# Performance work log

Hardware: AMD Instinct MI355X
Metric: run time of the kernel (lower is better)

## Reference

```python
import jax, jax.numpy as jnp
import numpy as np

N = 20000          # graph_size
IN_DIM = 256
H, D = 3, 64       # num_heads (hardcoded 3 in source), out_dim
E = 640000         # N * avg_degree(32)
NEG_SLOPE = 0.2    # DGL GATConv default negative_slope


def setup_inputs() -> dict:
    key = jax.random.key(0)
    ks = jax.random.split(key, 8)
    feat = jax.random.normal(ks[0], (N, IN_DIM), dtype=jnp.float32)
    W = jax.random.normal(ks[1], (IN_DIM, H * D), dtype=jnp.float32) * 0.05
    attn_l = jax.random.normal(ks[2], (H, D), dtype=jnp.float32) * 0.05
    attn_r = jax.random.normal(ks[3], (H, D), dtype=jnp.float32) * 0.05
    gat_bias = jnp.zeros((H * D,), dtype=jnp.float32)
    fc_w = jax.random.normal(ks[4], (N * H * D, 2), dtype=jnp.float32) * 0.001
    fc_b = jnp.zeros((2,), dtype=jnp.float32)
    src = jax.random.randint(ks[5], (E,), 0, N, dtype=jnp.int64)
    dst = jax.random.randint(ks[6], (E,), 0, N, dtype=jnp.int64)
    return {"feat": feat, "W": W, "attn_l": attn_l, "attn_r": attn_r,
            "gat_bias": gat_bias, "fc_w": fc_w, "fc_b": fc_b,
            "src": src, "dst": dst}


def reference(feat, W, attn_l, attn_r, gat_bias, fc_w, fc_b, src, dst):
    n = feat.shape[0]
    # GATConv: projected multi-head features [N, H, D]
    h = (feat @ W).reshape(n, H, D)
    el = jnp.einsum('nhd,hd->nh', h, attn_l)   # [N, H]
    er = jnp.einsum('nhd,hd->nh', h, attn_r)   # [N, H]
    # per-edge raw attention logits, LeakyReLU(el[src] + er[dst])
    e = jax.nn.leaky_relu(el[src] + er[dst], negative_slope=NEG_SLOPE)  # [E, H]
    # edge-softmax grouped by destination node (stable)
    m = jax.ops.segment_max(e, dst, num_segments=n)   # [N, H]
    ex = jnp.exp(e - m[dst])
    denom = jax.ops.segment_sum(ex, dst, num_segments=n)  # [N, H]
    alpha = ex / denom[dst]                            # [E, H]
    # weighted message aggregation: out[v] = sum_{(u->v)} alpha * h[u]
    msg = h[src] * alpha[:, :, None]                   # [E, H, D]
    out = jax.ops.segment_sum(msg, dst, num_segments=n)  # [N, H, D]
    out = out + gat_bias.reshape(H, D)                 # GATConv bias
    out = jax.nn.relu(out)                             # self.activation
    # Flatten(start_dim=0) -> Linear(N*H*D, 2)
    return out.reshape(-1) @ fc_w + fc_b               # [2]
```

## Files before the change

### kernel.cpp

```cpp
#include <hip/hip_runtime.h>
#include <hip/hip_bf16.h>
#include <cstdint>
#include <cstddef>

#define INDIM  256
#define HD     192
#define NHEADS 3
#define NEG_SLOPE 0.2f
#define ELLPAD 96
#define LPAD   97
#define CSHIFT 7
#define NBUCK  160
#define BCAP   4608
#define FNODES 16
#define P1CHUNK 2048

typedef __attribute__((ext_vector_type(8))) short short8;
typedef __attribute__((ext_vector_type(4))) float f32x4;

__device__ __forceinline__ float wave_sum(float v) {
#pragma unroll
    for (int o = 32; o; o >>= 1) v += __shfl_xor(v, o, 64);
    return v;
}

__global__ __launch_bounds__(256) void prep_kernel(
    const float* __restrict__ W, __hip_bfloat16* __restrict__ Wt,
    int* __restrict__ gCur)
{
    const int b = blockIdx.x, tid = threadIdx.x;
    if (b == 0) {
        if (tid < NBUCK) gCur[tid] = 0;
        return;
    }
    int n = b - 1;
    Wt[n * 256 + tid] = __float2bfloat16(W[tid * HD + n]);
}

__global__ __launch_bounds__(256) void gemm_bucket_kernel(
    const float* __restrict__ feat,
    const __hip_bfloat16* __restrict__ Wt,
    const float* __restrict__ attn_l, const float* __restrict__ attn_r,
    __hip_bfloat16* __restrict__ hb, float* __restrict__ el,
    float* __restrict__ er, int M,
    const int* __restrict__ src, const int* __restrict__ dst,
    int* __restrict__ gCur, int2* __restrict__ pairs,
    int E, int gemmBlocks)
{
    const int tid = threadIdx.x;
    if (blockIdx.x >= gemmBlocks) {
        __shared__ int cnt[NBUCK];
        __shared__ int base[NBUCK];
        const int e0 = (blockIdx.x - gemmBlocks) * P1CHUNK;
        if (tid < NBUCK) cnt[tid] = 0;
        __syncthreads();
        int d[8], s[8], b[8], l[8];
#pragma unroll
        for (int u = 0; u < 8; u++) {
            int e = e0 + u * 256 + tid;
            if (e < E) {
                d[u] = dst[e]; s[u] = src[e];
                b[u] = d[u] >> CSHIFT;
                l[u] = atomicAdd(&cnt[b[u]], 1);
            } else b[u] = -1;
        }
        __syncthreads();
        if (tid < NBUCK && cnt[tid] > 0) base[tid] = atomicAdd(&gCur[tid], cnt[tid]);
        __syncthreads();
#pragma unroll
        for (int u = 0; u < 8; u++) {
            if (b[u] >= 0) {
                int idx = base[b[u]] + l[u];
                if (idx < BCAP)
                    pairs[(size_t)b[u] * BCAP + idx] = make_int2(d[u], s[u]);
            }
        }
        return;
    }
    __shared__ __hip_bfloat16 As[64][40];
    __shared__ __hip_bfloat16 Bs[192][40];
    const int lane = tid & 63, w = tid >> 6;
    const int q = lane >> 4, ll = lane & 15;
    const int row0 = blockIdx.x * 64;

    f32x4 acc[12];
#pragma unroll
    for (int c = 0; c < 12; c++) acc[c] = (f32x4){0.f, 0.f, 0.f, 0.f};

    const int sr = tid >> 2, sk = (tid & 3) * 8;
    const int grow = row0 + sr;
    const bool arow = grow < M;
    const float* ap = feat + (size_t)grow * INDIM + sk;
    const __hip_bfloat16* bp = Wt + (size_t)tid * INDIM;

    float4 a0 = make_float4(0.f, 0.f, 0.f, 0.f), a1 = a0;
    if (arow) { a0 = *(const float4*)ap; a1 = *(const float4*)(ap + 4); }
    uint4 b0, b1, b2, b3;
    if (tid < HD) {
        b0 = *(const uint4*)(bp);      b1 = *(const uint4*)(bp + 8);
        b2 = *(const uint4*)(bp + 16); b3 = *(const uint4*)(bp + 24);
    }

    for (int k0 = 0; k0 < INDIM; k0 += 32) {
        __hip_bfloat16 ab[8] = {__float2bfloat16(a0.x), __float2bfloat16(a0.y),
                                __float2bfloat16(a0.z), __float2bfloat16(a0.w),
                                __float2bfloat16(a1.x), __float2bfloat16(a1.y),
                                __float2bfloat16(a1.z), __float2bfloat16(a1.w)};
        __syncthreads();
        *(uint4*)&As[sr][sk] = *(const uint4*)ab;
        if (tid < HD) {
            *(uint4*)&Bs[tid][0]  = b0;
            *(uint4*)&Bs[tid][8]  = b1;
            *(uint4*)&Bs[tid][16] = b2;
            *(uint4*)&Bs[tid][24] = b3;
        }
        if (k0 + 32 < INDIM) {
            if (arow) {
                a0 = *(const float4*)(ap + k0 + 32);
                a1 = *(const float4*)(ap + k0 + 36);
            }
            if (tid < HD) {
                const __hip_bfloat16* bq = bp + k0 + 32;
                b0 = *(const uint4*)(bq);      b1 = *(const uint4*)(bq + 8);
                b2 = *(const uint4*)(bq + 16); b3 = *(const uint4*)(bq + 24);
            }
        }
        __syncthreads();

        short8 af = *(const short8*)&As[w * 16 + ll][q * 8];
#pragma unroll
        for (int c = 0; c < 12; c++) {
            short8 bf = *(const short8*)&Bs[c * 16 + ll][q * 8];
            acc[c] = __builtin_amdgcn_mfma_f32_16x16x32_bf16(af, bf, acc[c], 0, 0, 0);
        }
    }

    float al[12], ar[12];
#pragma unroll
    for (int c = 0; c < 12; c++) {
        al[c] = attn_l[c * 16 + ll];
        ar[c] = attn_r[c * 16 + ll];
    }
    float sl[3][4], sr_[3][4];
#pragma unroll
    for (int hd = 0; hd < 3; hd++)
#pragma unroll
        for (int i = 0; i < 4; i++) {
            float a = 0.f, b = 0.f;
#pragma unroll
            for (int f = 0; f < 4; f++) {
                a = fmaf(acc[hd * 4 + f][i], al[hd * 4 + f], a);
                b = fmaf(acc[hd * 4 + f][i], ar[hd * 4 + f], b);
            }
            sl[hd][i] = a; sr_[hd][i] = b;
        }
#pragma unroll
    for (int hd = 0; hd < 3; hd++)
#pragma unroll
        for (int i = 0; i < 4; i++)
#pragma unroll
            for (int off = 1; off < 16; off <<= 1) {
                sl[hd][i]  += __shfl_xor(sl[hd][i],  off, 64);
                sr_[hd][i] += __shfl_xor(sr_[hd][i], off, 64);
            }
#pragma unroll
    for (int c = 0; c < 12; c++)
#pragma unroll
        for (int i = 0; i < 4; i++) {
            int row = row0 + w * 16 + q * 4 + i;
            if (row < M)
                hb[(size_t)row * HD + c * 16 + ll] = __float2bfloat16(acc[c][i]);
        }
    if (ll == 0) {
#pragma unroll
        for (int i = 0; i < 4; i++) {
            int row = row0 + w * 16 + q * 4 + i;
            if (row < M) {
#pragma unroll
                for (int hd = 0; hd < 3; hd++) {
                    el[row * 4 + hd] = sl[hd][i];
                    er[row * 4 + hd] = sr_[hd][i];
                }
            }
        }
    }
}

__global__ __launch_bounds__(1024) void gat_bucket_kernel(
    const __hip_bfloat16* __restrict__ h, const float* __restrict__ el,
    const float* __restrict__ er, const int2* __restrict__ pairs,
    const int* __restrict__ gCur, const float* __restrict__ gbias,
    const float* __restrict__ fc_w, float* __restrict__ pA,
    float* __restrict__ pB, int N)
{
    __shared__ int cur[FNODES];
    __shared__ int lell[FNODES][LPAD];
    __shared__ float4 sE[16][64];

    const int bid = blockIdx.x;
    const int tid = threadIdx.x;
    const int lane = tid & 63, wslot = tid >> 6;
    const int cb = bid >> 3, sub = bid & 7;

    if (tid < FNODES) cur[tid] = 0;
    __syncthreads();
    const int pcnt = min(gCur[cb], BCAP);
    const int2* pp = pairs + (size_t)cb * BCAP;
    for (int i = tid; i < pcnt; i += 1024) {
        int2 p = pp[i];
        int nl = p.x & 127;
        if ((nl >> 4) == sub) {
            int f = nl & 15;
            int r = atomicAdd(&cur[f], 1);
            if (r < ELLPAD) lell[f][r] = p.y;
        }
    }
    __syncthreads();

    const int v = bid * FNODES + wslot;
    if (v >= N) return;

    const int cnt = min(cur[wslot], ELLPAD);
    const int* rowp = &lell[wslot][0];
    const float4 erv = ((const float4*)er)[v];
    const float er0 = erv.x, er1 = erv.y, er2 = erv.z;
    const __hip_bfloat16* hl = h + lane;

    float acc0 = 0.f, acc1 = 0.f, acc2 = 0.f;
    float d0 = 0.f, d1 = 0.f, d2 = 0.f;

    for (int chunk = 0; chunk < cnt; chunk += 64) {
        const int i = chunk + lane;
        float w0 = 0.f, w1 = 0.f, w2 = 0.f;
        int s = 0;
        if (i < cnt) {
            s = rowp[i];
            const float4 le = ((const float4*)el)[s];
            float l0 = le.x + er0;
            float l1 = le.y + er1;
            float l2 = le.z + er2;
            l0 = l0 > 0.f ? l0 : NEG_SLOPE * l0;
            l1 = l1 > 0.f ? l1 : NEG_SLOPE * l1;
            l2 = l2 > 0.f ? l2 : NEG_SLOPE * l2;
            w0 = __expf(l0); w1 = __expf(l1); w2 = __expf(l2);
        }
        d0 += w0; d1 += w1; d2 += w2;
        sE[wslot][lane] = make_float4(__int_as_float(s), w0, w1, w2);
        __asm__ volatile("s_waitcnt lgkmcnt(0)" ::: "memory");

        const int rem = min(cnt - chunk, 64);
        const int nR = (rem + 7) & ~7;
        for (int j = 0; j < nR; j += 8) {
            float4 e[8];
#pragma unroll
            for (int u = 0; u < 8; u++) e[u] = sE[wslot][j + u];
            float x0[8], x1[8], x2[8];
#pragma unroll
            for (int u = 0; u < 8; u++) {
                const __hip_bfloat16* p = hl + (size_t)__float_as_int(e[u].x) * HD;
                x0[u] = __bfloat162float(p[0]);
                x1[u] = __bfloat162float(p[64]);
                x2[u] = __bfloat162float(p[128]);
            }
#pragma unroll
            for (int u = 0; u < 8; u++) {
                acc0 = fmaf(e[u].y, x0[u], acc0);
                acc1 = fmaf(e[u].z, x1[u], acc1);
                acc2 = fmaf(e[u].w, x2[u], acc2);
            }
        }
    }

    d0 = wave_sum(d0); d1 = wave_sum(d1); d2 = wave_sum(d2);

    float o0 = (d0 > 0.f) ? acc0 / d0 : 0.f;
    float o1 = (d1 > 0.f) ? acc1 / d1 : 0.f;
    float o2 = (d2 > 0.f) ? acc2 / d2 : 0.f;
    o0 = fmaxf(o0 + gbias[lane], 0.f);
    o1 = fmaxf(o1 + gbias[64 + lane], 0.f);
    o2 = fmaxf(o2 + gbias[128 + lane], 0.f);

    const size_t bidx = (size_t)v * HD;
    float2 w0v = ((const float2*)fc_w)[bidx + lane];
    float2 w1v = ((const float2*)fc_w)[bidx + 64 + lane];
    float2 w2v = ((const float2*)fc_w)[bidx + 128 + lane];
    float f0 = fmaf(o0, w0v.x, fmaf(o1, w1v.x, o2 * w2v.x));
    float f1 = fmaf(o0, w0v.y, fmaf(o1, w1v.y, o2 * w2v.y));

    f0 = wave_sum(f0); f1 = wave_sum(f1);
    if (lane == 0) { pA[v] = f0; pB[v] = f1; }
}

__global__ __launch_bounds__(1024) void final_reduce(const float* __restrict__ pA,
                                                     const float* __restrict__ pB,
                                                     const float* __restrict__ fc_b,
                                                     float* __restrict__ out, int nb)
{
    int tid = threadIdx.x;
    float s0 = 0.f, s1 = 0.f;
    for (int i = tid; i < nb; i += 1024) { s0 += pA[i]; s1 += pB[i]; }
    s0 = wave_sum(s0); s1 = wave_sum(s1);
    __shared__ float sh[32];
    int lane = tid & 63, w = tid >> 6;
    if (lane == 0) { sh[w * 2] = s0; sh[w * 2 + 1] = s1; }
    __syncthreads();
    if (tid == 0) {
        float t0 = 0.f, t1 = 0.f;
#pragma unroll
        for (int i = 0; i < 16; i++) { t0 += sh[i * 2]; t1 += sh[i * 2 + 1]; }
        out[0] = t0 + fc_b[0];
        out[1] = t1 + fc_b[1];
    }
}

extern "C" void kernel_launch(void* const* d_in, const int* in_sizes, int n_in,
                              void* d_out, int out_size, void* d_ws, size_t ws_size,
                              hipStream_t stream)
{
    const float* feat   = (const float*)d_in[0];
    const float* W      = (const float*)d_in[1];
    const float* attn_l = (const float*)d_in[2];
    const float* attn_r = (const float*)d_in[3];
    const float* gbias  = (const float*)d_in[4];
    const float* fc_w   = (const float*)d_in[5];
    const float* fc_b   = (const float*)d_in[6];
    const int*   src    = (const int*)d_in[7];
    const int*   dst    = (const int*)d_in[8];

    const int N = in_sizes[0] / INDIM;
    const int E = in_sizes[7];
    const int nFine = (N + FNODES - 1) / FNODES;

    __hip_bfloat16* Wt = (__hip_bfloat16*)d_ws;
    __hip_bfloat16* hb = Wt + HD * INDIM;
    float* el = (float*)(hb + (size_t)N * HD);
    float* er = el + (size_t)N * 4;
    int* gCur = (int*)(er + (size_t)N * 4);
    int2* pairs = (int2*)(gCur + NBUCK);
    float* pA = (float*)(pairs + (size_t)NBUCK * BCAP);
    float* pB = pA + N;

    prep_kernel<<<1 + HD, 256, 0, stream>>>(W, Wt, gCur);

    const int gemmBlocks = (N + 63) / 64;
    const int p1Blocks = (E + P1CHUNK - 1) / P1CHUNK;
    gemm_bucket_kernel<<<gemmBlocks + p1Blocks, 256, 0, stream>>>(
        feat, Wt, attn_l, attn_r, hb, el, er, N,
        src, dst, gCur, pairs, E, gemmBlocks);

    gat_bucket_kernel<<<nFine, 1024, 0, stream>>>(hb, el, er, pairs, gCur,
                                                  gbias, fc_w, pA, pB, N);
    final_reduce<<<1, 1024, 0, stream>>>(pA, pB, fc_b, (float*)d_out, N);
}
```

Before: 165.5 us.

## Pack edge pairs into 32-bit words and widen gather unroll in GAT kernel

Each edge is now stored in the bucket buffer as a single 32-bit word, source index shifted left by 7 with the low 7 bits of the destination, instead of an int2. The aggregation kernel reads these words four at a time with uint4 loads and keeps the shared-memory adjacency list as 16-bit indices. This halves the bucket write and re-read traffic, which matters because each bucket is scanned by eight blocks. The fc_w loads are issued before the edge loop to hide their latency, and the feature gather is unrolled to 16 raw bf16 loads per step. The 16-bit adjacency indices only hold node ids below 65536, and the wider unroll raises register pressure.

```diff
diff --git a/kernel.cpp b/kernel.cpp
--- a/kernel.cpp
+++ b/kernel.cpp
@@ -8,7 +8,6 @@
 #define NHEADS 3
 #define NEG_SLOPE 0.2f
 #define ELLPAD 96
-#define LPAD   97
 #define CSHIFT 7
 #define NBUCK  160
 #define BCAP   4608
@@ -22,6 +21,12 @@
 #pragma unroll
     for (int o = 32; o; o >>= 1) v += __shfl_xor(v, o, 64);
     return v;
+}
+
+__device__ __forceinline__ float bfu(unsigned short u) {
+    __hip_bfloat16 b;
+    *(unsigned short*)&b = u;
+    return __bfloat162float(b);
 }
 
 __global__ __launch_bounds__(256) void prep_kernel(
@@ -44,7 +49,7 @@
     __hip_bfloat16* __restrict__ hb, float* __restrict__ el,
     float* __restrict__ er, int M,
     const int* __restrict__ src, const int* __restrict__ dst,
-    int* __restrict__ gCur, int2* __restrict__ pairs,
+    int* __restrict__ gCur, unsigned int* __restrict__ pairs,
     int E, int gemmBlocks)
 {
     const int tid = threadIdx.x;
@@ -72,7 +77,8 @@
             if (b[u] >= 0) {
                 int idx = base[b[u]] + l[u];
                 if (idx < BCAP)
-                    pairs[(size_t)b[u] * BCAP + idx] = make_int2(d[u], s[u]);
+                    pairs[(size_t)b[u] * BCAP + idx] =
+                        ((unsigned int)s[u] << 7) | (unsigned int)(d[u] & 127);
             }
         }
         return;
@@ -188,13 +194,13 @@
 
 __global__ __launch_bounds__(1024) void gat_bucket_kernel(
     const __hip_bfloat16* __restrict__ h, const float* __restrict__ el,
-    const float* __restrict__ er, const int2* __restrict__ pairs,
+    const float* __restrict__ er, const unsigned int* __restrict__ pairs,
     const int* __restrict__ gCur, const float* __restrict__ gbias,
     const float* __restrict__ fc_w, float* __restrict__ pA,
     float* __restrict__ pB, int N)
 {
     __shared__ int cur[FNODES];
-    __shared__ int lell[FNODES][LPAD];
+    __shared__ unsigned short lell[FNODES][ELLPAD];
     __shared__ float4 sE[16][64];
 
     const int bid = blockIdx.x;
@@ -205,14 +211,20 @@
     if (tid < FNODES) cur[tid] = 0;
     __syncthreads();
     const int pcnt = min(gCur[cb], BCAP);
-    const int2* pp = pairs + (size_t)cb * BCAP;
-    for (int i = tid; i < pcnt; i += 1024) {
-        int2 p = pp[i];
-        int nl = p.x & 127;
-        if ((nl >> 4) == sub) {
-            int f = nl & 15;
-            int r = atomicAdd(&cur[f], 1);
-            if (r < ELLPAD) lell[f][r] = p.y;
+    const unsigned int* pp = pairs + (size_t)cb * BCAP;
+    for (int i4 = tid * 4; i4 < pcnt; i4 += 4096) {
+        uint4 pk = *(const uint4*)(pp + i4);
+#pragma unroll
+        for (int k = 0; k < 4; k++) {
+            if (i4 + k < pcnt) {
+                unsigned int p = (&pk.x)[k];
+                int nl = (int)(p & 127u);
+                if ((nl >> 4) == sub) {
+                    int f = nl & 15;
+                    int r = atomicAdd(&cur[f], 1);
+                    if (r < ELLPAD) lell[f][r] = (unsigned short)(p >> 7);
+                }
+            }
         }
     }
     __syncthreads();
@@ -221,10 +233,15 @@
     if (v >= N) return;
 
     const int cnt = min(cur[wslot], ELLPAD);
-    const int* rowp = &lell[wslot][0];
+    const unsigned short* rowp = &lell[wslot][0];
     const float4 erv = ((const float4*)er)[v];
     const float er0 = erv.x, er1 = erv.y, er2 = erv.z;
     const __hip_bfloat16* hl = h + lane;
+
+    const size_t bidx = (size_t)v * HD;
+    const float2 w0v = ((const float2*)fc_w)[bidx + lane];
+    const float2 w1v = ((const float2*)fc_w)[bidx + 64 + lane];
+    const float2 w2v = ((const float2*)fc_w)[bidx + 128 + lane];
 
     float acc0 = 0.f, acc1 = 0.f, acc2 = 0.f;
     float d0 = 0.f, d1 = 0.f, d2 = 0.f;
@@ -234,7 +251,7 @@
         float w0 = 0.f, w1 = 0.f, w2 = 0.f;
         int s = 0;
         if (i < cnt) {
-            s = rowp[i];
+            s = (int)rowp[i];
             const float4 le = ((const float4*)el)[s];
             float l0 = le.x + er0;
             float l1 = le.y + er1;
@@ -249,24 +266,24 @@
         __asm__ volatile("s_waitcnt lgkmcnt(0)" ::: "memory");
 
         const int rem = min(cnt - chunk, 64);
-        const int nR = (rem + 7) & ~7;
-        for (int j = 0; j < nR; j += 8) {
-            float4 e[8];
-#pragma unroll
-            for (int u = 0; u < 8; u++) e[u] = sE[wslot][j + u];
-            float x0[8], x1[8], x2[8];
-#pragma unroll
-            for (int u = 0; u < 8; u++) {
-                const __hip_bfloat16* p = hl + (size_t)__float_as_int(e[u].x) * HD;
-                x0[u] = __bfloat162float(p[0]);
-                x1[u] = __bfloat162float(p[64]);
-                x2[u] = __bfloat162float(p[128]);
-            }
-#pragma unroll
-            for (int u = 0; u < 8; u++) {
-                acc0 = fmaf(e[u].y, x0[u], acc0);
-                acc1 = fmaf(e[u].z, x1[u], acc1);
-                acc2 = fmaf(e[u].w, x2[u], acc2);
+        const int nR = (rem + 15) & ~15;
+        for (int j = 0; j < nR; j += 16) {
+            unsigned short y0[16], y1[16], y2[16];
+#pragma unroll
+            for (int u = 0; u < 16; u++) {
+                const int sg = __float_as_int(sE[wslot][j + u].x);
+                const unsigned short* p =
+                    (const unsigned short*)(hl + (size_t)sg * HD);
+                y0[u] = p[0];
+                y1[u] = p[64];
+                y2[u] = p[128];
+            }
+#pragma unroll
+            for (int u = 0; u < 16; u++) {
+                const float4 e = sE[wslot][j + u];
+                acc0 = fmaf(e.y, bfu(y0[u]), acc0);
+                acc1 = fmaf(e.z, bfu(y1[u]), acc1);
+                acc2 = fmaf(e.w, bfu(y2[u]), acc2);
             }
         }
     }
@@ -280,10 +297,6 @@
     o1 = fmaxf(o1 + gbias[64 + lane], 0.f);
     o2 = fmaxf(o2 + gbias[128 + lane], 0.f);
 
-    const size_t bidx = (size_t)v * HD;
-    float2 w0v = ((const float2*)fc_w)[bidx + lane];
-    float2 w1v = ((const float2*)fc_w)[bidx + 64 + lane];
-    float2 w2v = ((const float2*)fc_w)[bidx + 128 + lane];
     float f0 = fmaf(o0, w0v.x, fmaf(o1, w1v.x, o2 * w2v.x));
     float f1 = fmaf(o0, w0v.y, fmaf(o1, w1v.y, o2 * w2v.y));
 
@@ -336,7 +349,7 @@
     float* el = (float*)(hb + (size_t)N * HD);
     float* er = el + (size_t)N * 4;
     int* gCur = (int*)(er + (size_t)N * 4);
-    int2* pairs = (int2*)(gCur + NBUCK);
+    unsigned int* pairs = (unsigned int*)(gCur + NBUCK);
     float* pA = (float*)(pairs + (size_t)NBUCK * BCAP);
     float* pB = pA + N;
 
```

After: 170.1 us. 1.03x slower.

## Pack edge pairs to 32-bit, shrink GAT blocks, fuse final reduction via last-block

Applied to the files above, without the earlier changes.

Edge bucket entries are packed into one 32-bit word (source id shifted left by 7, plus the low 7 bits of the destination), which halves the pairs write and read traffic. Source ids are stored as ushort in the LDS ELL table. The aggregation kernel now uses 256-thread blocks where each wave handles 4 nodes in turn, and blocks are ordered so consecutive blocks read different buckets. The final_reduce launch is removed: a global atomic counter picks the last block to finish, and that block sums the partials. This saves one launch but adds a serial tail reduction and a fence-based handoff between blocks.

```diff
diff --git a/kernel.cpp b/kernel.cpp
--- a/kernel.cpp
+++ b/kernel.cpp
@@ -8,11 +8,9 @@
 #define NHEADS 3
 #define NEG_SLOPE 0.2f
 #define ELLPAD 96
-#define LPAD   97
 #define CSHIFT 7
 #define NBUCK  160
 #define BCAP   4608
-#define FNODES 16
 #define P1CHUNK 2048
 
 typedef __attribute__((ext_vector_type(8))) short short8;
@@ -26,11 +24,12 @@
 
 __global__ __launch_bounds__(256) void prep_kernel(
     const float* __restrict__ W, __hip_bfloat16* __restrict__ Wt,
-    int* __restrict__ gCur)
+    int* __restrict__ gCur, int* __restrict__ gDone)
 {
     const int b = blockIdx.x, tid = threadIdx.x;
     if (b == 0) {
         if (tid < NBUCK) gCur[tid] = 0;
+        if (tid == NBUCK) *gDone = 0;
         return;
     }
     int n = b - 1;
@@ -44,7 +43,7 @@
     __hip_bfloat16* __restrict__ hb, float* __restrict__ el,
     float* __restrict__ er, int M,
     const int* __restrict__ src, const int* __restrict__ dst,
-    int* __restrict__ gCur, int2* __restrict__ pairs,
+    int* __restrict__ gCur, unsigned int* __restrict__ pairs,
     int E, int gemmBlocks)
 {
     const int tid = threadIdx.x;
@@ -72,7 +71,8 @@
             if (b[u] >= 0) {
                 int idx = base[b[u]] + l[u];
                 if (idx < BCAP)
-                    pairs[(size_t)b[u] * BCAP + idx] = make_int2(d[u], s[u]);
+                    pairs[(size_t)b[u] * BCAP + idx] =
+                        ((unsigned int)s[u] << 7) | (unsigned int)(d[u] & 127);
             }
         }
         return;
@@ -186,128 +186,146 @@
     }
 }
 
-__global__ __launch_bounds__(1024) void gat_bucket_kernel(
+__global__ __launch_bounds__(256) void gat_bucket_kernel(
     const __hip_bfloat16* __restrict__ h, const float* __restrict__ el,
-    const float* __restrict__ er, const int2* __restrict__ pairs,
+    const float* __restrict__ er, const unsigned int* __restrict__ pairs,
     const int* __restrict__ gCur, const float* __restrict__ gbias,
-    const float* __restrict__ fc_w, float* __restrict__ pA,
-    float* __restrict__ pB, int N)
+    const float* __restrict__ fc_w, const float* __restrict__ fc_b,
+    float* __restrict__ pA, float* __restrict__ pB,
+    float* __restrict__ out, int* __restrict__ gDone, int N)
 {
-    __shared__ int cur[FNODES];
-    __shared__ int lell[FNODES][LPAD];
-    __shared__ float4 sE[16][64];
+    __shared__ int cur[16];
+    __shared__ unsigned short lell[16][ELLPAD];
+    __shared__ float4 sE[4][64];
+    __shared__ int isLast;
+    __shared__ float sh[8];
 
     const int bid = blockIdx.x;
     const int tid = threadIdx.x;
     const int lane = tid & 63, wslot = tid >> 6;
-    const int cb = bid >> 3, sub = bid & 7;
-
-    if (tid < FNODES) cur[tid] = 0;
+    const int cb = bid % NBUCK, sub = bid / NBUCK;
+
+    if (tid < 16) cur[tid] = 0;
     __syncthreads();
     const int pcnt = min(gCur[cb], BCAP);
-    const int2* pp = pairs + (size_t)cb * BCAP;
-    for (int i = tid; i < pcnt; i += 1024) {
-        int2 p = pp[i];
-        int nl = p.x & 127;
-        if ((nl >> 4) == sub) {
-            int f = nl & 15;
-            int r = atomicAdd(&cur[f], 1);
-            if (r < ELLPAD) lell[f][r] = p.y;
-        }
-    }
-    __syncthreads();
-
-    const int v = bid * FNODES + wslot;
-    if (v >= N) return;
-
-    const int cnt = min(cur[wslot], ELLPAD);
-    const int* rowp = &lell[wslot][0];
-    const float4 erv = ((const float4*)er)[v];
-    const float er0 = erv.x, er1 = erv.y, er2 = erv.z;
+    const unsigned int* pp = pairs + (size_t)cb * BCAP;
+    for (int i4 = tid * 4; i4 < pcnt; i4 += 1024) {
+        uint4 pk = *(const uint4*)(pp + i4);
+#pragma unroll
+        for (int k = 0; k < 4; k++) {
+            if (i4 + k < pcnt) {
+                unsigned int p = (&pk.x)[k];
+                int nl = (int)(p & 127u);
+                if ((nl >> 4) == sub) {
+                    int f = nl & 15;
+                    int r = atomicAdd(&cur[f], 1);
+                    if (r < ELLPAD) lell[f][r] = (unsigned short)(p >> 7);
+                }
+            }
+        }
+    }
+    __syncthreads();
+
     const __hip_bfloat16* hl = h + lane;
 
-    float acc0 = 0.f, acc1 = 0.f, acc2 = 0.f;
-    float d0 = 0.f, d1 = 0.f, d2 = 0.f;
-
-    for (int chunk = 0; chunk < cnt; chunk += 64) {
-        const int i = chunk + lane;
-        float w0 = 0.f, w1 = 0.f, w2 = 0.f;
-        int s = 0;
-        if (i < cnt) {
-            s = rowp[i];
-            const float4 le = ((const float4*)el)[s];
-            float l0 = le.x + er0;
-            float l1 = le.y + er1;
-            float l2 = le.z + er2;
-            l0 = l0 > 0.f ? l0 : NEG_SLOPE * l0;
-            l1 = l1 > 0.f ? l1 : NEG_SLOPE * l1;
-            l2 = l2 > 0.f ? l2 : NEG_SLOPE * l2;
-            w0 = __expf(l0); w1 = __expf(l1); w2 = __expf(l2);
-        }
-        d0 += w0; d1 += w1; d2 += w2;
-        sE[wslot][lane] = make_float4(__int_as_float(s), w0, w1, w2);
-        __asm__ volatile("s_waitcnt lgkmcnt(0)" ::: "memory");
-
-        const int rem = min(cnt - chunk, 64);
-        const int nR = (rem + 7) & ~7;
-        for (int j = 0; j < nR; j += 8) {
-            float4 e[8];
-#pragma unroll
-            for (int u = 0; u < 8; u++) e[u] = sE[wslot][j + u];
-            float x0[8], x1[8], x2[8];
-#pragma unroll
-            for (int u = 0; u < 8; u++) {
-                const __hip_bfloat16* p = hl + (size_t)__float_as_int(e[u].x) * HD;
-                x0[u] = __bfloat162float(p[0]);
-                x1[u] = __bfloat162float(p[64]);
-                x2[u] = __bfloat162float(p[128]);
-            }
-#pragma unroll
-            for (int u = 0; u < 8; u++) {
-                acc0 = fmaf(e[u].y, x0[u], acc0);
-                acc1 = fmaf(e[u].z, x1[u], acc1);
-                acc2 = fmaf(e[u].w, x2[u], acc2);
-            }
-        }
-    }
-
-    d0 = wave_sum(d0); d1 = wave_sum(d1); d2 = wave_sum(d2);
-
-    float o0 = (d0 > 0.f) ? acc0 / d0 : 0.f;
-    float o1 = (d1 > 0.f) ? acc1 / d1 : 0.f;
-    float o2 = (d2 > 0.f) ? acc2 / d2 : 0.f;
-    o0 = fmaxf(o0 + gbias[lane], 0.f);
-    o1 = fmaxf(o1 + gbias[64 + lane], 0.f);
-    o2 = fmaxf(o2 + gbias[128 + lane], 0.f);
-
-    const size_t bidx = (size_t)v * HD;
-    float2 w0v = ((const float2*)fc_w)[bidx + lane];
-    float2 w1v = ((const float2*)fc_w)[bidx + 64 + lane];
-    float2 w2v = ((const float2*)fc_w)[bidx + 128 + lane];
-    float f0 = fmaf(o0, w0v.x, fmaf(o1, w1v.x, o2 * w2v.x));
-    float f1 = fmaf(o0, w0v.y, fmaf(o1, w1v.y, o2 * w2v.y));
-
-    f0 = wave_sum(f0); f1 = wave_sum(f1);
-    if (lane == 0) { pA[v] = f0; pB[v] = f1; }
-}
-
-__global__ __launch_bounds__(1024) void final_reduce(const float* __restrict__ pA,
-                                                     const float* __restrict__ pB,
-                                                     const float* __restrict__ fc_b,
-                                                     float* __restrict__ out, int nb)
-{
-    int tid = threadIdx.x;
+#pragma unroll 1
+    for (int k = 0; k < 4; k++) {
+        const int f = (wslot << 2) + k;
+        const int v = cb * 128 + sub * 16 + f;
+        if (v >= N) continue;
+
+        const int cnt = min(cur[f], ELLPAD);
+        const unsigned short* rowp = &lell[f][0];
+        const float4 erv = ((const float4*)er)[v];
+        const float er0 = erv.x, er1 = erv.y, er2 = erv.z;
+
+        float acc0 = 0.f, acc1 = 0.f, acc2 = 0.f;
+        float d0 = 0.f, d1 = 0.f, d2 = 0.f;
+
+        for (int chunk = 0; chunk < cnt; chunk += 64) {
+            const int i = chunk + lane;
+            float w0 = 0.f, w1 = 0.f, w2 = 0.f;
+            int s = 0;
+            if (i < cnt) {
+                s = (int)rowp[i];
+                const float4 le = ((const float4*)el)[s];
+                float l0 = le.x + er0;
+                float l1 = le.y + er1;
+                float l2 = le.z + er2;
+                l0 = l0 > 0.f ? l0 : NEG_SLOPE * l0;
+                l1 = l1 > 0.f ? l1 : NEG_SLOPE * l1;
+                l2 = l2 > 0.f ? l2 : NEG_SLOPE * l2;
+                w0 = __expf(l0); w1 = __expf(l1); w2 = __expf(l2);
+            }
+            d0 += w0; d1 += w1; d2 += w2;
+            sE[wslot][lane] = make_float4(__int_as_float(s), w0, w1, w2);
+            __asm__ volatile("s_waitcnt lgkmcnt(0)" ::: "memory");
+
+            const int rem = min(cnt - chunk, 64);
+            const int nR = (rem + 7) & ~7;
+            for (int j = 0; j < nR; j += 8) {
+                float4 e[8];
+#pragma unroll
+                for (int u = 0; u < 8; u++) e[u] = sE[wslot][j + u];
+                float x0[8], x1[8], x2[8];
+#pragma unroll
+                for (int u = 0; u < 8; u++) {
+                    const __hip_bfloat16* p = hl + (size_t)__float_as_int(e[u].x) * HD;
+                    x0[u] = __bfloat162float(p[0]);
+                    x1[u] = __bfloat162float(p[64]);
+                    x2[u] = __bfloat162float(p[128]);
+                }
+#pragma unroll
+                for (int u = 0; u < 8; u++) {
+                    acc0 = fmaf(e[u].y, x0[u], acc0);
+                    acc1 = fmaf(e[u].z, x1[u], acc1);
+                    acc2 = fmaf(e[u].w, x2[u], acc2);
+                }
+            }
+        }
+
+        d0 = wave_sum(d0); d1 = wave_sum(d1); d2 = wave_sum(d2);
+
+        float o0 = (d0 > 0.f) ? acc0 / d0 : 0.f;
+        float o1 = (d1 > 0.f) ? acc1 / d1 : 0.f;
+        float o2 = (d2 > 0.f) ? acc2 / d2 : 0.f;
+        o0 = fmaxf(o0 + gbias[lane], 0.f);
+        o1 = fmaxf(o1 + gbias[64 + lane], 0.f);
+        o2 = fmaxf(o2 + gbias[128 + lane], 0.f);
+
+        const size_t bidx = (size_t)v * HD;
+        float2 w0v = ((const float2*)fc_w)[bidx + lane];
+        float2 w1v = ((const float2*)fc_w)[bidx + 64 + lane];
+        float2 w2v = ((const float2*)fc_w)[bidx + 128 + lane];
+        float f0 = fmaf(o0, w0v.x, fmaf(o1, w1v.x, o2 * w2v.x));
+        float f1 = fmaf(o0, w0v.y, fmaf(o1, w1v.y, o2 * w2v.y));
+
+        f0 = wave_sum(f0); f1 = wave_sum(f1);
+        if (lane == 0) { pA[v] = f0; pB[v] = f1; }
+    }
+
+    __syncthreads();
+    __threadfence();
+    if (tid == 0) {
+        int done = atomicAdd(gDone, 1);
+        isLast = (done == (int)gridDim.x - 1);
+    }
+    __syncthreads();
+    if (!isLast) return;
+
+    __threadfence();
     float s0 = 0.f, s1 = 0.f;
-    for (int i = tid; i < nb; i += 1024) { s0 += pA[i]; s1 += pB[i]; }
+    for (int i = tid; i < N; i += 256) {
+        s0 += __hip_atomic_load(&pA[i], __ATOMIC_RELAXED, __HIP_MEMORY_SCOPE_AGENT);
+        s1 += __hip_atomic_load(&pB[i], __ATOMIC_RELAXED, __HIP_MEMORY_SCOPE_AGENT);
+    }
     s0 = wave_sum(s0); s1 = wave_sum(s1);
-    __shared__ float sh[32];
-    int lane = tid & 63, w = tid >> 6;
-    if (lane == 0) { sh[w * 2] = s0; sh[w * 2 + 1] = s1; }
+    if (lane == 0) { sh[wslot * 2] = s0; sh[wslot * 2 + 1] = s1; }
     __syncthreads();
     if (tid == 0) {
         float t0 = 0.f, t1 = 0.f;
 #pragma unroll
-        for (int i = 0; i < 16; i++) { t0 += sh[i * 2]; t1 += sh[i * 2 + 1]; }
+        for (int i = 0; i < 4; i++) { t0 += sh[i * 2]; t1 += sh[i * 2 + 1]; }
         out[0] = t0 + fc_b[0];
         out[1] = t1 + fc_b[1];
     }
@@ -329,18 +347,18 @@
 
     const int N = in_sizes[0] / INDIM;
     const int E = in_sizes[7];
-    const int nFine = (N + FNODES - 1) / FNODES;
 
     __hip_bfloat16* Wt = (__hip_bfloat16*)d_ws;
     __hip_bfloat16* hb = Wt + HD * INDIM;
     float* el = (float*)(hb + (size_t)N * HD);
     float* er = el + (size_t)N * 4;
     int* gCur = (int*)(er + (size_t)N * 4);
-    int2* pairs = (int2*)(gCur + NBUCK);
+    unsigned int* pairs = (unsigned int*)(gCur + NBUCK);
     float* pA = (float*)(pairs + (size_t)NBUCK * BCAP);
     float* pB = pA + N;
-
-    prep_kernel<<<1 + HD, 256, 0, stream>>>(W, Wt, gCur);
+    int* gDone = (int*)(pB + N);
+
+    prep_kernel<<<1 + HD, 256, 0, stream>>>(W, Wt, gCur, gDone);
 
     const int gemmBlocks = (N + 63) / 64;
     const int p1Blocks = (E + P1CHUNK - 1) / P1CHUNK;
@@ -348,7 +366,8 @@
         feat, Wt, attn_l, attn_r, hb, el, er, N,
         src, dst, gCur, pairs, E, gemmBlocks);
 
-    gat_bucket_kernel<<<nFine, 1024, 0, stream>>>(hb, el, er, pairs, gCur,
-                                                  gbias, fc_w, pA, pB, N);
-    final_reduce<<<1, 1024, 0, stream>>>(pA, pB, fc_b, (float*)d_out, N);
-}
+    gat_bucket_kernel<<<NBUCK * 8, 256, 0, stream>>>(hb, el, er, pairs, gCur,
+                                                     gbias, fc_w, fc_b,
+                                                     pA, pB, (float*)d_out,
+                                                     gDone, N);
+}
```

After: 294.7 us. +78.1%, slower.
